# Optimization experiments

Measured on AMD Instinct MI355X. Metric: run time of the kernel, lower is better.

Reference implementation:

```python
import jax, jax.numpy as jnp
import numpy as np

D_MODEL = 2048
NUM_HEADS = 16
D_K = D_MODEL // NUM_HEADS  # 128, per-head dim used for RoPE
ROPE_THETA = 10000.0
MAX_SEQ_LEN = 2048
BATCH = 4
SEQ = 2048


def _trunc_normal(key, shape, std):
    # approximate trunc_normal_(mean=0, std, a=-3std, b=3std)
    return jnp.clip(std * jax.random.normal(key, shape), -3 * std, 3 * std)


def setup_inputs() -> dict:
    key = jax.random.key(0)
    ks = jax.random.split(key, 6)
    x = jax.random.normal(ks[0], (BATCH, SEQ, D_MODEL), dtype=jnp.float32)
    token_positions = jnp.arange(SEQ, dtype=jnp.int32)
    std = float(np.sqrt(2.0 / (D_MODEL + D_MODEL)))
    wq = _trunc_normal(ks[1], (D_MODEL, D_MODEL), std)  # (d_out, d_in)
    wk = _trunc_normal(ks[2], (D_MODEL, D_MODEL), std)
    wv = _trunc_normal(ks[3], (D_MODEL, D_MODEL), std)
    wo = _trunc_normal(ks[4], (D_MODEL, D_MODEL), std)
    return {"x": x, "token_positions": token_positions,
            "wq": wq, "wk": wk, "wv": wv, "wo": wo}


def _rope(t, pos):
    # t: (b, h, n, d_k), pos: (n,) int
    # interleaved pairs: (x1, x2) = (t[..., 0::2], t[..., 1::2])
    freqs = 1.0 / (ROPE_THETA ** (jnp.arange(0, D_K, 2, dtype=jnp.float32) / D_K))
    angles = pos.astype(jnp.float32)[:, None] * freqs[None, :]  # (n, d_k/2)
    cos = jnp.cos(angles).astype(t.dtype)
    sin = jnp.sin(angles).astype(t.dtype)
    tr = t.reshape(*t.shape[:-1], D_K // 2, 2)
    x1, x2 = tr[..., 0], tr[..., 1]
    y1 = cos * x1 - sin * x2
    y2 = sin * x1 + cos * x2
    return jnp.stack([y1, y2], axis=-1).reshape(t.shape)


def reference(x, token_positions, wq, wk, wv, wo):
    b, n, d = x.shape
    q = jnp.einsum('bnd,od->bno', x, wq)
    k = jnp.einsum('bnd,od->bno', x, wk)
    v = jnp.einsum('bnd,od->bno', x, wv)
    # split heads for RoPE: (b, n, h*dk) -> (b, h, n, dk)
    split = lambda t: t.reshape(b, n, NUM_HEADS, D_K).transpose(0, 2, 1, 3)
    merge = lambda t: t.transpose(0, 2, 1, 3).reshape(b, n, d)
    q = merge(_rope(split(q), token_positions))
    k = merge(_rope(split(k), token_positions))
    # NOTE: source merges heads back BEFORE flash attention -> single-head
    # attention over full d_model with causal mask, scale 1/sqrt(d_model)
    scale = 1.0 / jnp.sqrt(jnp.asarray(d, dtype=x.dtype))
    scores = jnp.einsum('bqd,bkd->bqk', q, k) * scale  # (b, n, n)
    causal = jnp.tril(jnp.ones((n, n), dtype=bool))
    scores = jnp.where(causal[None, :, :], scores, jnp.finfo(scores.dtype).min)
    attn = jax.nn.softmax(scores, axis=-1)
    out = jnp.einsum('bqk,bkd->bqd', attn, v)
    return jnp.einsum('bnd,od->bno', out, wo)
```

## Files before the change

kernel.cpp:

```cpp
#include <hip/hip_runtime.h>
#include <hip/hip_bf16.h>
#include <cstdint>
#include <cmath>

typedef __attribute__((ext_vector_type(4))) float f32x4;
typedef __attribute__((ext_vector_type(8))) short bf16x8;

#define BAR()   __builtin_amdgcn_s_barrier()
#define PRIO1() __builtin_amdgcn_s_setprio(1)
#define PRIO0() __builtin_amdgcn_s_setprio(0)
#define WAITV2() asm volatile("s_waitcnt vmcnt(2)" ::: "memory")
#define WAITV0() asm volatile("s_waitcnt vmcnt(0)" ::: "memory")
#define MM(a,b,c) __builtin_amdgcn_mfma_f32_16x16x32_bf16((a),(b),(c),0,0,0)

__device__ __forceinline__ void gl_lds16(const __hip_bfloat16* g, char* l) {
    __builtin_amdgcn_global_load_lds(
        (const __attribute__((address_space(1))) void*)g,
        (__attribute__((address_space(3))) void*)l, 16, 0, 0);
}
__device__ __forceinline__ void store_c(float* C, size_t i, float v) { C[i] = v; }
__device__ __forceinline__ void store_c(__hip_bfloat16* C, size_t i, float v) { C[i] = __float2bfloat16(v); }

#define LDA_(mi,kk) (*(const bf16x8*)(dA + ((((wr8+(mi))<<1)+(kk))<<10) + rswz))
#define LDB_(ni,kk) (*(const bf16x8*)(dB + ((((wc4+(ni))<<1)+(kk))<<10) + rswz))
#define ST_(s) do{ if((s)<4) gl_lds16(Asrc + (size_t)((s)*64)*lda + ktn, nA + (s)*8192 + wbase); \
                   else      gl_lds16(Bsrc + (size_t)(((s)-4)*64)*ldb + ktn, nB + ((s)-4)*8192 + wbase); }while(0)
#define PH_LOADA(mih) do{ _Pragma("unroll") for(int i_=0;i_<4;++i_){ af[i_][0]=LDA_((mih)*4+i_,0); af[i_][1]=LDA_((mih)*4+i_,1);} }while(0)
#define PH_LOADB(nih) do{ _Pragma("unroll") for(int i_=0;i_<2;++i_){ bfr[i_][0]=LDB_((nih)*2+i_,0); bfr[i_][1]=LDB_((nih)*2+i_,1);} }while(0)
#define PH_MMA(mih,nih) do{ _Pragma("unroll") for(int i_=0;i_<4;++i_){ _Pragma("unroll") for(int j_=0;j_<2;++j_){ \
    f32x4 c_=acc[(mih)*4+i_][(nih)*2+j_]; c_=MM(af[i_][0],bfr[j_][0],c_); c_=MM(af[i_][1],bfr[j_][1],c_); acc[(mih)*4+i_][(nih)*2+j_]=c_; } } }while(0)

#define TILEB(DA,DB,NA,NB) do{ \
    const char* dA=(DA); const char* dB=(DB); char* nA=(NA); char* nB=(NB); \
    if (pf) { ST_(0); ST_(1); WAITV2(); } else { WAITV0(); } \
    BAR(); \
    PH_LOADA(0); PH_LOADB(0); \
    PRIO1(); PH_MMA(0,0); PRIO0(); BAR(); \
    if (pf) { ST_(2); ST_(3); } \
    PH_LOADB(1); \
    BAR(); PRIO1(); PH_MMA(0,1); PRIO0(); BAR(); \
    if (pf) { ST_(4); ST_(5); } \
    PH_LOADA(1); \
    BAR(); PRIO1(); PH_MMA(1,1); PRIO0(); BAR(); \
    if (pf) { ST_(6); ST_(7); } \
    PH_LOADB(0); \
    BAR(); PRIO1(); PH_MMA(1,0); PRIO0(); BAR(); \
}while(0)

template<typename CT, bool CSKIP, bool KLIM>
__global__ __launch_bounds__(512, 2)
void gemm256(const __hip_bfloat16* __restrict__ A, const __hip_bfloat16* __restrict__ B,
             CT* __restrict__ C, int K, int lda, int ldb, int ldc, int nbx,
             float alpha, size_t sA, size_t sB, size_t sC)
{
    __shared__ char lds[131072];
    char* const lA0 = lds;
    char* const lB0 = lds + 32768;
    char* const lA1 = lds + 65536;
    char* const lB1 = lds + 98304;

    const int nwg = gridDim.x;
    const int q8 = nwg >> 3, r8 = nwg & 7;
    const int xcd = blockIdx.x & 7, blk = blockIdx.x >> 3;
    const int wg = (xcd < r8 ? xcd * (q8 + 1) : r8 * (q8 + 1) + (xcd - r8) * q8) + blk;
    const int bx = wg % nbx, by = wg / nbx;
    const int bm0 = by * 256, bn0 = bx * 256;
    if (CSKIP && bn0 >= bm0 + 256) return;

    A += sA * blockIdx.y; B += sB * blockIdx.y; C += sC * blockIdx.y;

    const int tid  = threadIdx.x;
    const int lane = tid & 63;
    const int w    = tid >> 6;
    const int wr8  = (w >> 2) * 8;
    const int wc4  = (w & 3) * 4;
    const int wbase = w * 1024;

    const int pq  = lane * 16;
    const int uq  = pq ^ (((pq >> 9) & 1) << 5);
    const int sr0 = (w >> 1) * 16 + (uq >> 6);
    const int sc0 = (w & 1) * 32 + ((uq & 63) >> 1);
    const __hip_bfloat16* Asrc = A + (size_t)(bm0 + sr0) * lda + sc0;
    const __hip_bfloat16* Bsrc = B + (size_t)(bn0 + sr0) * ldb + sc0;

    const int rb   = (lane & 15) * 64 + (lane >> 4) * 16;
    const int rswz = rb ^ (((rb >> 9) & 1) << 5);

    f32x4 acc[8][4] = {};
    bf16x8 af[4][2], bfr[2][2];

    const int klim = bm0 + 256;
    const int kend = KLIM ? (K < klim ? K : klim) : K;
    const int nt   = kend >> 6;

    {
        char* nA = lA0; char* nB = lB0; const int ktn = 0;
        ST_(0); ST_(1); ST_(2); ST_(3); ST_(4); ST_(5); ST_(6); ST_(7);
    }
    for (int t = 0; t < nt; t += 2) {
        {   const bool pf = (t + 1 < nt); const int ktn = (t + 1) << 6;
            TILEB(lA0, lB0, lA1, lB1);
        }
        {   const bool pf = (t + 2 < nt); const int ktn = (t + 2) << 6;
            TILEB(lA1, lB1, lA0, lB0);
        }
    }

    const int cr = (lane >> 4) * 4, cc = lane & 15;
    const int wrow = bm0 + (w >> 2) * 128, wcol = bn0 + (w & 3) * 64;
#pragma unroll
    for (int mi = 0; mi < 8; ++mi)
#pragma unroll
        for (int ni = 0; ni < 4; ++ni) {
            const int row = wrow + mi * 16 + cr;
            const int col = wcol + ni * 16 + cc;
#pragma unroll
            for (int j = 0; j < 4; ++j)
                store_c(C, (size_t)(row + j) * ldc + col, acc[mi][ni][j] * alpha);
        }
}

__global__ void f32_to_bf16_vec(const float* __restrict__ in,
                                __hip_bfloat16* __restrict__ out, int n4)
{
    int i = blockIdx.x * 256 + threadIdx.x;
    if (i >= n4) return;
    float4 v = ((const float4*)in)[i];
    union { ushort4 u; __hip_bfloat16 h[4]; } o;
    o.h[0] = __float2bfloat16(v.x);
    o.h[1] = __float2bfloat16(v.y);
    o.h[2] = __float2bfloat16(v.z);
    o.h[3] = __float2bfloat16(v.w);
    ((ushort4*)out)[i] = o.u;
}

__global__ void rope_table(const int* __restrict__ pos, float2* __restrict__ tab, int N)
{
    int i = blockIdx.x * 256 + threadIdx.x;
    if (i >= N * 64) return;
    int n = i >> 6, j = i & 63;
    float p = (float)pos[n];
    float ang = p * powf(10000.f, -(float)j * (1.0f / 64.0f));
    tab[i] = make_float2(cosf(ang), sinf(ang));
}

__global__ void rope_apply(__hip_bfloat16* __restrict__ T,
                           const float2* __restrict__ tab, int total)
{
    int i = blockIdx.x * 256 + threadIdx.x;
    if (i >= total) return;
    int r  = i >> 10;
    int pr = i & 1023;
    int n  = r & 2047;
    int j  = pr & 63;
    float2 cs = tab[(n << 6) + j];
    __hip_bfloat162* p = (__hip_bfloat162*)(T + ((size_t)r << 11) + (pr << 1));
    __hip_bfloat162 v = *p;
    float x1 = __bfloat162float(v.x);
    float x2 = __bfloat162float(v.y);
    v.x = __float2bfloat16(cs.x * x1 - cs.y * x2);
    v.y = __float2bfloat16(cs.y * x1 + cs.x * x2);
    *p = v;
}

__global__ void softmax_causal_ip(float* __restrict__ S, int N)
{
    const int q = blockIdx.x;
    float* srow = S + ((size_t)blockIdx.y * N + q) * N;
    __shared__ float buf[2048];
    __shared__ float red[8];
    const int tid = threadIdx.x;

    float4* b4 = (float4*)buf;
    const float4* s4 = (const float4*)srow;
    for (int i = tid; i < N / 4; i += 256) b4[i] = s4[i];
    __syncthreads();

    float m = -1e30f;
    for (int j = tid; j <= q; j += 256) m = fmaxf(m, buf[j]);
#pragma unroll
    for (int o = 32; o > 0; o >>= 1) m = fmaxf(m, __shfl_xor(m, o));
    if ((tid & 63) == 0) red[tid >> 6] = m;
    __syncthreads();
    m = fmaxf(fmaxf(red[0], red[1]), fmaxf(red[2], red[3]));

    float sum = 0.f;
    for (int j = tid; j <= q; j += 256) { float e = __expf(buf[j] - m); buf[j] = e; sum += e; }
#pragma unroll
    for (int o = 32; o > 0; o >>= 1) sum += __shfl_xor(sum, o);
    if ((tid & 63) == 0) red[4 + (tid >> 6)] = sum;
    __syncthreads();
    const float inv = 1.f / (red[4] + red[5] + red[6] + red[7]);

    __hip_bfloat162* p2 = (__hip_bfloat162*)srow;
    for (int i = tid; i < N / 2; i += 256) {
        int j0 = i * 2;
        __hip_bfloat162 h;
        h.x = __float2bfloat16(j0     <= q ? buf[j0]     * inv : 0.f);
        h.y = __float2bfloat16(j0 + 1 <= q ? buf[j0 + 1] * inv : 0.f);
        p2[i] = h;
    }
}

__global__ void transpose_bf16(const __hip_bfloat16* __restrict__ V,
                               __hip_bfloat16* __restrict__ Vt, int N)
{
    __shared__ __hip_bfloat16 tile[32][33];
    const size_t bo = (size_t)blockIdx.z * N * N;
    const int k0 = blockIdx.x * 32, d0 = blockIdx.y * 32;
    const int tx = threadIdx.x, ty = threadIdx.y;
#pragma unroll
    for (int j = 0; j < 4; ++j)
        tile[ty + 8 * j][tx] = V[bo + (size_t)(k0 + ty + 8 * j) * N + d0 + tx];
    __syncthreads();
#pragma unroll
    for (int j = 0; j < 4; ++j)
        Vt[bo + (size_t)(d0 + ty + 8 * j) * N + k0 + tx] = tile[tx][ty + 8 * j];
}

extern "C" void kernel_launch(void* const* d_in, const int* in_sizes, int n_in,
                              void* d_out, int out_size, void* d_ws, size_t ws_size,
                              hipStream_t stream)
{
    const float* x  = (const float*)d_in[0];
    const int* pos  = (const int*)d_in[1];
    const float* wq = (const float*)d_in[2];
    const float* wk = (const float*)d_in[3];
    const float* wv = (const float*)d_in[4];
    const float* wo = (const float*)d_in[5];
    float* out = (float*)d_out;

    const int B = 4, N = 2048, D = 2048;
    const int M = B * N;
    const size_t MB = 1ull << 20;
    if (ws_size < 192 * MB) return;

    char* w = (char*)d_ws;
    __hip_bfloat16* Qb  = (__hip_bfloat16*)(w + 0 * MB);
    __hip_bfloat16* Kb  = (__hip_bfloat16*)(w + 32 * MB);
    __hip_bfloat16* Vb  = (__hip_bfloat16*)(w + 64 * MB);
    __hip_bfloat16* wqb = (__hip_bfloat16*)(w + 96 * MB);
    __hip_bfloat16* wkb = (__hip_bfloat16*)(w + 104 * MB);
    __hip_bfloat16* wvb = (__hip_bfloat16*)(w + 112 * MB);
    __hip_bfloat16* wob = (__hip_bfloat16*)(w + 120 * MB);
    __hip_bfloat16* xb  = (__hip_bfloat16*)(w + 128 * MB);
    __hip_bfloat16* Vt  = xb;
    __hip_bfloat16* AO  = (__hip_bfloat16*)(w + 160 * MB);

    float2* tab = (float2*)wqb;
    float*  Sal = (float*)d_out;

    f32_to_bf16_vec<<<(M * D / 4 + 255) / 256, 256, 0, stream>>>(x,  xb,  M * D / 4);
    f32_to_bf16_vec<<<(D * D / 4 + 255) / 256, 256, 0, stream>>>(wq, wqb, D * D / 4);
    f32_to_bf16_vec<<<(D * D / 4 + 255) / 256, 256, 0, stream>>>(wk, wkb, D * D / 4);
    f32_to_bf16_vec<<<(D * D / 4 + 255) / 256, 256, 0, stream>>>(wv, wvb, D * D / 4);
    f32_to_bf16_vec<<<(D * D / 4 + 255) / 256, 256, 0, stream>>>(wo, wob, D * D / 4);

    const int nbxP = D / 256;
    dim3 gp((D / 256) * (M / 256), 1);
    gemm256<__hip_bfloat16, false, false><<<gp, 512, 0, stream>>>(xb, wqb, Qb, D, D, D, D, nbxP, 1.f, 0, 0, 0);
    gemm256<__hip_bfloat16, false, false><<<gp, 512, 0, stream>>>(xb, wkb, Kb, D, D, D, D, nbxP, 1.f, 0, 0, 0);
    gemm256<__hip_bfloat16, false, false><<<gp, 512, 0, stream>>>(xb, wvb, Vb, D, D, D, D, nbxP, 1.f, 0, 0, 0);

    rope_table<<<(N * 64 + 255) / 256, 256, 0, stream>>>(pos, tab, N);
    rope_apply<<<(M * 1024 + 255) / 256, 256, 0, stream>>>(Qb, tab, M * 1024);
    rope_apply<<<(M * 1024 + 255) / 256, 256, 0, stream>>>(Kb, tab, M * 1024);

    transpose_bf16<<<dim3(N / 32, N / 32, B), dim3(32, 8), 0, stream>>>(Vb, Vt, N);

    const float scale = 1.0f / sqrtf((float)D);
    const int nbxA = N / 256;
    dim3 ga(nbxA * (N / 256), B);
    gemm256<float, true, false><<<ga, 512, 0, stream>>>(
        Qb, Kb, Sal, D, D, D, N, nbxA, scale, (size_t)N * D, (size_t)N * D, (size_t)N * N);
    softmax_causal_ip<<<dim3(N, B), 256, 0, stream>>>(Sal, N);
    gemm256<__hip_bfloat16, false, true><<<ga, 512, 0, stream>>>(
        (const __hip_bfloat16*)Sal, Vt, AO, N, 2 * N, D, D, nbxA, 1.f,
        (size_t)2 * N * N, (size_t)N * D, (size_t)N * D);

    gemm256<float, false, false><<<gp, 512, 0, stream>>>(AO, wob, out, D, D, D, D, nbxP, 1.f, 0, 0, 0);
}
```

Measured before the change: 479.8 us.

## Restructure GEMM to triple-buffered 32-wide K pipeline and batch small kernels

The 256x256 GEMM mainloop goes from double-buffered 64-wide K tiles to a triple-buffered ring of 32-wide K tiles, using 96KB of LDS instead of 128KB. Each iteration has two compute phases that overlap the next-next prefetch, with fewer barriers per tile. Separately, the four weight conversions merge into one launch, the two RoPE applies merge into one vectorized launch handling 8 elements per thread, and the rope table moves to its own workspace slot computed early. The aim is to raise MFMA overlap and cut launch and memory overhead, at the cost of more loop iterations and more complex LDS indexing.

```diff
diff --git a/kernel.cpp b/kernel.cpp
--- a/kernel.cpp
+++ b/kernel.cpp
@@ -9,7 +9,7 @@
 #define BAR()   __builtin_amdgcn_s_barrier()
 #define PRIO1() __builtin_amdgcn_s_setprio(1)
 #define PRIO0() __builtin_amdgcn_s_setprio(0)
-#define WAITV2() asm volatile("s_waitcnt vmcnt(2)" ::: "memory")
+#define WAITV4() asm volatile("s_waitcnt vmcnt(4)" ::: "memory")
 #define WAITV0() asm volatile("s_waitcnt vmcnt(0)" ::: "memory")
 #define MM(a,b,c) __builtin_amdgcn_mfma_f32_16x16x32_bf16((a),(b),(c),0,0,0)
 
@@ -21,31 +21,10 @@
 __device__ __forceinline__ void store_c(float* C, size_t i, float v) { C[i] = v; }
 __device__ __forceinline__ void store_c(__hip_bfloat16* C, size_t i, float v) { C[i] = __float2bfloat16(v); }
 
-#define LDA_(mi,kk) (*(const bf16x8*)(dA + ((((wr8+(mi))<<1)+(kk))<<10) + rswz))
-#define LDB_(ni,kk) (*(const bf16x8*)(dB + ((((wc4+(ni))<<1)+(kk))<<10) + rswz))
-#define ST_(s) do{ if((s)<4) gl_lds16(Asrc + (size_t)((s)*64)*lda + ktn, nA + (s)*8192 + wbase); \
-                   else      gl_lds16(Bsrc + (size_t)(((s)-4)*64)*ldb + ktn, nB + ((s)-4)*8192 + wbase); }while(0)
-#define PH_LOADA(mih) do{ _Pragma("unroll") for(int i_=0;i_<4;++i_){ af[i_][0]=LDA_((mih)*4+i_,0); af[i_][1]=LDA_((mih)*4+i_,1);} }while(0)
-#define PH_LOADB(nih) do{ _Pragma("unroll") for(int i_=0;i_<2;++i_){ bfr[i_][0]=LDB_((nih)*2+i_,0); bfr[i_][1]=LDB_((nih)*2+i_,1);} }while(0)
-#define PH_MMA(mih,nih) do{ _Pragma("unroll") for(int i_=0;i_<4;++i_){ _Pragma("unroll") for(int j_=0;j_<2;++j_){ \
-    f32x4 c_=acc[(mih)*4+i_][(nih)*2+j_]; c_=MM(af[i_][0],bfr[j_][0],c_); c_=MM(af[i_][1],bfr[j_][1],c_); acc[(mih)*4+i_][(nih)*2+j_]=c_; } } }while(0)
-
-#define TILEB(DA,DB,NA,NB) do{ \
-    const char* dA=(DA); const char* dB=(DB); char* nA=(NA); char* nB=(NB); \
-    if (pf) { ST_(0); ST_(1); WAITV2(); } else { WAITV0(); } \
-    BAR(); \
-    PH_LOADA(0); PH_LOADB(0); \
-    PRIO1(); PH_MMA(0,0); PRIO0(); BAR(); \
-    if (pf) { ST_(2); ST_(3); } \
-    PH_LOADB(1); \
-    BAR(); PRIO1(); PH_MMA(0,1); PRIO0(); BAR(); \
-    if (pf) { ST_(4); ST_(5); } \
-    PH_LOADA(1); \
-    BAR(); PRIO1(); PH_MMA(1,1); PRIO0(); BAR(); \
-    if (pf) { ST_(6); ST_(7); } \
-    PH_LOADB(0); \
-    BAR(); PRIO1(); PH_MMA(1,0); PRIO0(); BAR(); \
-}while(0)
+#define STAGEA(nb, kt) do{ gl_lds16(Asrc + (kt),                        lds + (nb)         + wb); \
+                           gl_lds16(Asrc + (size_t)128 * lda + (kt),    lds + (nb) +  8192 + wb);}while(0)
+#define STAGEB(nb, kt) do{ gl_lds16(Bsrc + (kt),                        lds + (nb) + 16384 + wb); \
+                           gl_lds16(Bsrc + (size_t)128 * ldb + (kt),    lds + (nb) + 24576 + wb);}while(0)
 
 template<typename CT, bool CSKIP, bool KLIM>
 __global__ __launch_bounds__(512, 2)
@@ -53,11 +32,7 @@
              CT* __restrict__ C, int K, int lda, int ldb, int ldc, int nbx,
              float alpha, size_t sA, size_t sB, size_t sC)
 {
-    __shared__ char lds[131072];
-    char* const lA0 = lds;
-    char* const lB0 = lds + 32768;
-    char* const lA1 = lds + 65536;
-    char* const lB1 = lds + 98304;
+    __shared__ __align__(1024) char lds[98304];
 
     const int nwg = gridDim.x;
     const int q8 = nwg >> 3, r8 = nwg & 7;
@@ -72,38 +47,64 @@
     const int tid  = threadIdx.x;
     const int lane = tid & 63;
     const int w    = tid >> 6;
-    const int wr8  = (w >> 2) * 8;
-    const int wc4  = (w & 3) * 4;
-    const int wbase = w * 1024;
-
-    const int pq  = lane * 16;
-    const int uq  = pq ^ (((pq >> 9) & 1) << 5);
-    const int sr0 = (w >> 1) * 16 + (uq >> 6);
-    const int sc0 = (w & 1) * 32 + ((uq & 63) >> 1);
-    const __hip_bfloat16* Asrc = A + (size_t)(bm0 + sr0) * lda + sc0;
-    const __hip_bfloat16* Bsrc = B + (size_t)(bn0 + sr0) * ldb + sc0;
+    const int wb   = w * 1024;
 
     const int rb   = (lane & 15) * 64 + (lane >> 4) * 16;
     const int rswz = rb ^ (((rb >> 9) & 1) << 5);
+    const int srA  = (w >> 2) * 8;
+    const int srB  = (w & 3) * 4;
+
+    const int q0 = tid * 16;
+    const int uq = q0 ^ (((q0 >> 9) & 1) << 5);
+    const int r0 = ((q0 >> 10) << 4) | ((uq >> 6) & 15);
+    const int c0 = (uq & 63) >> 1;
+    const __hip_bfloat16* Asrc = A + (size_t)(bm0 + r0) * lda + c0;
+    const __hip_bfloat16* Bsrc = B + (size_t)(bn0 + r0) * ldb + c0;
 
     f32x4 acc[8][4] = {};
-    bf16x8 af[4][2], bfr[2][2];
+    bf16x8 af[4], bf[4];
 
     const int klim = bm0 + 256;
     const int kend = KLIM ? (K < klim ? K : klim) : K;
-    const int nt   = kend >> 6;
-
-    {
-        char* nA = lA0; char* nB = lB0; const int ktn = 0;
-        ST_(0); ST_(1); ST_(2); ST_(3); ST_(4); ST_(5); ST_(6); ST_(7);
-    }
-    for (int t = 0; t < nt; t += 2) {
-        {   const bool pf = (t + 1 < nt); const int ktn = (t + 1) << 6;
-            TILEB(lA0, lB0, lA1, lB1);
-        }
-        {   const bool pf = (t + 2 < nt); const int ktn = (t + 2) << 6;
-            TILEB(lA1, lB1, lA0, lB0);
-        }
+    const int nt   = kend >> 5;
+
+    STAGEA(0, 0); STAGEB(0, 0);
+    if (nt > 1) { STAGEA(32768, 32); STAGEB(32768, 32); }
+
+    for (int t = 0; t < nt; ++t) {
+        if (t + 1 < nt) WAITV4(); else WAITV0();
+        BAR();
+        const char* dA = lds + (t % 3) * 32768;
+        const char* dB = dA + 16384;
+        const int  nbo = ((t + 2) % 3) * 32768;
+        const bool pf  = (t + 2 < nt);
+        const int  kt  = (t + 2) << 5;
+
+#pragma unroll
+        for (int i = 0; i < 4; ++i) af[i] = *(const bf16x8*)(dA + ((srA + i) << 10) + rswz);
+#pragma unroll
+        for (int i = 0; i < 4; ++i) bf[i] = *(const bf16x8*)(dB + ((srB + i) << 10) + rswz);
+        if (pf) STAGEA(nbo, kt);
+        BAR();
+        PRIO1();
+#pragma unroll
+        for (int mi = 0; mi < 4; ++mi)
+#pragma unroll
+            for (int ni = 0; ni < 4; ++ni)
+                acc[mi][ni] = MM(af[mi], bf[ni], acc[mi][ni]);
+        PRIO0();
+
+#pragma unroll
+        for (int i = 0; i < 4; ++i) af[i] = *(const bf16x8*)(dA + ((srA + 4 + i) << 10) + rswz);
+        if (pf) STAGEB(nbo, kt);
+        BAR();
+        PRIO1();
+#pragma unroll
+        for (int mi = 0; mi < 4; ++mi)
+#pragma unroll
+            for (int ni = 0; ni < 4; ++ni)
+                acc[4 + mi][ni] = MM(af[mi], bf[ni], acc[4 + mi][ni]);
+        PRIO0();
     }
 
     const int cr = (lane >> 4) * 4, cc = lane & 15;
@@ -134,6 +135,29 @@
     ((ushort4*)out)[i] = o.u;
 }
 
+__global__ void conv_w4(const float* __restrict__ w0, const float* __restrict__ w1,
+                        const float* __restrict__ w2, const float* __restrict__ w3,
+                        __hip_bfloat16* o0, __hip_bfloat16* o1,
+                        __hip_bfloat16* o2, __hip_bfloat16* o3, int n4)
+{
+    int i = blockIdx.x * 256 + threadIdx.x;
+    if (i >= n4) return;
+    const float* src; __hip_bfloat16* dst;
+    switch (blockIdx.y) {
+        case 0: src = w0; dst = o0; break;
+        case 1: src = w1; dst = o1; break;
+        case 2: src = w2; dst = o2; break;
+        default: src = w3; dst = o3; break;
+    }
+    float4 v = ((const float4*)src)[i];
+    union { ushort4 u; __hip_bfloat16 h[4]; } o;
+    o.h[0] = __float2bfloat16(v.x);
+    o.h[1] = __float2bfloat16(v.y);
+    o.h[2] = __float2bfloat16(v.z);
+    o.h[3] = __float2bfloat16(v.w);
+    ((ushort4*)dst)[i] = o.u;
+}
+
 __global__ void rope_table(const int* __restrict__ pos, float2* __restrict__ tab, int N)
 {
     int i = blockIdx.x * 256 + threadIdx.x;
@@ -144,23 +168,27 @@
     tab[i] = make_float2(cosf(ang), sinf(ang));
 }
 
-__global__ void rope_apply(__hip_bfloat16* __restrict__ T,
-                           const float2* __restrict__ tab, int total)
+__global__ void rope_apply2(__hip_bfloat16* __restrict__ Q, __hip_bfloat16* __restrict__ K,
+                            const float2* __restrict__ tab)
 {
     int i = blockIdx.x * 256 + threadIdx.x;
-    if (i >= total) return;
-    int r  = i >> 10;
-    int pr = i & 1023;
+    __hip_bfloat16* T = blockIdx.y ? K : Q;
+    int r  = i >> 8;
+    int cb = (i & 255) << 3;
     int n  = r & 2047;
-    int j  = pr & 63;
-    float2 cs = tab[(n << 6) + j];
-    __hip_bfloat162* p = (__hip_bfloat162*)(T + ((size_t)r << 11) + (pr << 1));
-    __hip_bfloat162 v = *p;
-    float x1 = __bfloat162float(v.x);
-    float x2 = __bfloat162float(v.y);
-    v.x = __float2bfloat16(cs.x * x1 - cs.y * x2);
-    v.y = __float2bfloat16(cs.y * x1 + cs.x * x2);
-    *p = v;
+    int j0 = (cb >> 1) & 63;
+    union { bf16x8 v; __hip_bfloat162 h[4]; } u;
+    __hip_bfloat16* p = T + ((size_t)r << 11) + cb;
+    u.v = *(const bf16x8*)p;
+#pragma unroll
+    for (int k = 0; k < 4; ++k) {
+        float2 cs = tab[(n << 6) + j0 + k];
+        float x1 = __bfloat162float(u.h[k].x);
+        float x2 = __bfloat162float(u.h[k].y);
+        u.h[k].x = __float2bfloat16(cs.x * x1 - cs.y * x2);
+        u.h[k].y = __float2bfloat16(cs.y * x1 + cs.x * x2);
+    }
+    *(bf16x8*)p = u.v;
 }
 
 __global__ void softmax_causal_ip(float* __restrict__ S, int N)
@@ -246,15 +274,14 @@
     __hip_bfloat16* xb  = (__hip_bfloat16*)(w + 128 * MB);
     __hip_bfloat16* Vt  = xb;
     __hip_bfloat16* AO  = (__hip_bfloat16*)(w + 160 * MB);
-
-    float2* tab = (float2*)wqb;
-    float*  Sal = (float*)d_out;
-
-    f32_to_bf16_vec<<<(M * D / 4 + 255) / 256, 256, 0, stream>>>(x,  xb,  M * D / 4);
-    f32_to_bf16_vec<<<(D * D / 4 + 255) / 256, 256, 0, stream>>>(wq, wqb, D * D / 4);
-    f32_to_bf16_vec<<<(D * D / 4 + 255) / 256, 256, 0, stream>>>(wk, wkb, D * D / 4);
-    f32_to_bf16_vec<<<(D * D / 4 + 255) / 256, 256, 0, stream>>>(wv, wvb, D * D / 4);
-    f32_to_bf16_vec<<<(D * D / 4 + 255) / 256, 256, 0, stream>>>(wo, wob, D * D / 4);
+    float2*         tab = (float2*)(w + 190 * MB);
+
+    float* Sal = (float*)d_out;
+
+    f32_to_bf16_vec<<<(M * D / 4 + 255) / 256, 256, 0, stream>>>(x, xb, M * D / 4);
+    conv_w4<<<dim3((D * D / 4 + 255) / 256, 4), 256, 0, stream>>>(
+        wq, wk, wv, wo, wqb, wkb, wvb, wob, D * D / 4);
+    rope_table<<<(N * 64 + 255) / 256, 256, 0, stream>>>(pos, tab, N);
 
     const int nbxP = D / 256;
     dim3 gp((D / 256) * (M / 256), 1);
@@ -262,9 +289,7 @@
     gemm256<__hip_bfloat16, false, false><<<gp, 512, 0, stream>>>(xb, wkb, Kb, D, D, D, D, nbxP, 1.f, 0, 0, 0);
     gemm256<__hip_bfloat16, false, false><<<gp, 512, 0, stream>>>(xb, wvb, Vb, D, D, D, D, nbxP, 1.f, 0, 0, 0);
 
-    rope_table<<<(N * 64 + 255) / 256, 256, 0, stream>>>(pos, tab, N);
-    rope_apply<<<(M * 1024 + 255) / 256, 256, 0, stream>>>(Qb, tab, M * 1024);
-    rope_apply<<<(M * 1024 + 255) / 256, 256, 0, stream>>>(Kb, tab, M * 1024);
+    rope_apply2<<<dim3(M * 256 / 256, 2), 256, 0, stream>>>(Qb, Kb, tab);
 
     transpose_bf16<<<dim3(N / 32, N / 32, B), dim3(32, 8), 0, stream>>>(Vb, Vt, N);
 
```

Result: slower. 491.9 us (+2.5%).
